# Performance work log

Hardware: AMD Instinct MI355X
Metric: run time of the kernel (lower is better)

The kernel has to match this reference:

```python
import jax, jax.numpy as jnp
import numpy as np

TOP_K = 2  # matches init_kwargs k

def setup_inputs() -> dict:
    key = jax.random.key(0)
    k1, k2 = jax.random.split(key)
    x = jax.random.normal(k1, (4, 4096, 2048), dtype=jnp.float32)
    gate_w = jax.random.normal(k2, (8, 2048), dtype=jnp.float32) * 0.02  # Linear weight [E, D]
    return {"x": x, "gate_w": gate_w}

def reference(x, gate_w):
    B, S, D = x.shape
    E = gate_w.shape[0]
    xf = x.reshape(-1, D)                              # [N, D], N = B*S
    gate_logits = jnp.einsum('nd,ed->ne', xf, gate_w)  # [N, E]
    probs = jax.nn.softmax(gate_logits.astype(jnp.float32), axis=-1)
    weights, selected = jax.lax.top_k(probs, TOP_K)    # [N, K], [N, K]
    weights = weights / jnp.sum(weights, axis=-1, keepdims=True)
    weights = weights.astype(x.dtype)
    # one_hot -> [N, K, E], permute(2,1,0) -> [E, K, N]
    expert_mask = jax.nn.one_hot(selected, E, dtype=jnp.int32).transpose(2, 1, 0)
    return weights, expert_mask, gate_logits
```

## Files before the change

### kernel.cpp

```cpp
#include <hip/hip_runtime.h>


constexpr int kN = 16384;
constexpr int kD = 2048;
constexpr int kE = 8;

__global__ __launch_bounds__(256, 4)
void moe_router_kernel(const float* __restrict__ x,
                       const float* __restrict__ gw,
                       float* __restrict__ out)
{
    const int lane = threadIdx.x & 63;
    const int wv   = threadIdx.x >> 6;
    const int n0   = blockIdx.x * 16 + wv * 4;

    const float* xr = x + (long)n0 * kD;

    float acc[4][8];
#pragma unroll
    for (int r = 0; r < 4; ++r)
#pragma unroll
        for (int e = 0; e < 8; ++e) acc[r][e] = 0.f;

#pragma unroll
    for (int it = 0; it < 8; ++it) {
        const int c = it * 256 + lane * 4;
        float4 g[8];
#pragma unroll
        for (int e = 0; e < 8; ++e)
            g[e] = *reinterpret_cast<const float4*>(gw + e * kD + c);
#pragma unroll
        for (int r = 0; r < 4; ++r) {
            const float4 xv = *reinterpret_cast<const float4*>(xr + r * kD + c);
#pragma unroll
            for (int e = 0; e < 8; ++e) {
                acc[r][e] = fmaf(xv.x, g[e].x, acc[r][e]);
                acc[r][e] = fmaf(xv.y, g[e].y, acc[r][e]);
                acc[r][e] = fmaf(xv.z, g[e].z, acc[r][e]);
                acc[r][e] = fmaf(xv.w, g[e].w, acc[r][e]);
            }
        }
    }

#pragma unroll
    for (int r = 0; r < 4; ++r)
#pragma unroll
        for (int e = 0; e < 8; ++e) {
            float v = acc[r][e];
            v += __shfl_xor(v, 1);
            v += __shfl_xor(v, 2);
            v += __shfl_xor(v, 4);
            v += __shfl_xor(v, 8);
            v += __shfl_xor(v, 16);
            v += __shfl_xor(v, 32);
            acc[r][e] = v;
        }

    float* out_w = out;
    float* out_m = out + 2 * kN;
    float* out_l = out + 2 * kN + 2 * kE * kN;

    auto load_row = [&](int r, float* le) {
#pragma unroll
        for (int e = 0; e < 8; ++e) {
            float v = acc[0][e];
            v = (r == 1) ? acc[1][e] : v;
            v = (r == 2) ? acc[2][e] : v;
            v = (r == 3) ? acc[3][e] : v;
            le[e] = v;
        }
    };
    auto top2 = [](const float* le, int& s0, int& s1) {
        float b0 = le[0]; s0 = 0;
#pragma unroll
        for (int e = 1; e < 8; ++e)
            if (le[e] > b0) { b0 = le[e]; s0 = e; }
        float b1 = -3.4e38f; s1 = (s0 == 0) ? 1 : 0;
#pragma unroll
        for (int e = 0; e < 8; ++e)
            if (e != s0 && le[e] > b1) { b1 = le[e]; s1 = e; }
    };

    {
        const int rm = lane & 3;
        const int km = (lane >> 2) & 1;
        const int em = lane >> 3;
        float le[8]; load_row(rm, le);
        int s0, s1; top2(le, s0, s1);
        const int sel = km ? s1 : s0;
        out_m[(long)em * (2 * kN) + (long)km * kN + (n0 + rm)] =
            (sel == em) ? 1.0f : 0.0f;
    }

    if (lane < 8) {
        const int rw = lane >> 1;
        const int kw = lane & 1;
        float le[8]; load_row(rw, le);
        int s0, s1; top2(le, s0, s1);
        float v0 = le[0], v1 = le[0];
#pragma unroll
        for (int e = 1; e < 8; ++e) {
            v0 = (e == s0) ? le[e] : v0;
            v1 = (e == s1) ? le[e] : v1;
        }
        const float d  = expf(v1 - v0);
        const float w0 = 1.0f / (1.0f + d);
        out_w[(long)(n0 + rw) * 2 + kw] = kw ? (d * w0) : w0;
    }

    if (lane < 32) {
        const int rl = lane >> 3;
        const int el = lane & 7;
        float le[8]; load_row(rl, le);
        float v = le[0];
#pragma unroll
        for (int e = 1; e < 8; ++e)
            v = (e == el) ? le[e] : v;
        out_l[(long)(n0 + rl) * 8 + el] = v;
    }
}

extern "C" void kernel_launch(void* const* d_in, const int* in_sizes, int n_in,
                              void* d_out, int out_size, void* d_ws, size_t ws_size,
                              hipStream_t stream)
{
    (void)in_sizes; (void)n_in; (void)d_ws; (void)ws_size; (void)out_size;
    const float* x  = (const float*)d_in[0];
    const float* gw = (const float*)d_in[1];
    float* out = (float*)d_out;

    dim3 grid(kN / 16);
    dim3 block(256);
    moe_router_kernel<<<grid, block, 0, stream>>>(x, gw, out);
}
```

Measured before the change: 37.97 us.

## Use nontemporal x loads, disable main-loop unroll, and transpose-reduce partial sums

The x rows are now loaded with nontemporal vector loads hoisted ahead of the gate-weight loads, and the main loop is no longer unrolled. The cross-lane reduction becomes a recursive-halving transpose that leaves each lane holding all 8 logits for one row, so the shuffle count drops and each lane computes top-2 only once. The aim is to cut shuffle/ALU overhead and cache pollution in this bandwidth-bound kernel. The rolled loop may expose load latency because fewer loads are in flight.

```diff
diff --git a/kernel.cpp b/kernel.cpp
--- a/kernel.cpp
+++ b/kernel.cpp
@@ -1,9 +1,12 @@
 #include <hip/hip_runtime.h>
+#include <math.h>
 
 
 constexpr int kN = 16384;
 constexpr int kD = 2048;
 constexpr int kE = 8;
+
+using f4 = __attribute__((ext_vector_type(4))) float;
 
 __global__ __launch_bounds__(256, 4)
 void moe_router_kernel(const float* __restrict__ x,
@@ -22,101 +25,94 @@
 #pragma unroll
         for (int e = 0; e < 8; ++e) acc[r][e] = 0.f;
 
-#pragma unroll
+#pragma unroll 1
     for (int it = 0; it < 8; ++it) {
         const int c = it * 256 + lane * 4;
-        float4 g[8];
+        f4 xv[4];
+#pragma unroll
+        for (int r = 0; r < 4; ++r)
+            xv[r] = __builtin_nontemporal_load(
+                reinterpret_cast<const f4*>(xr + (long)r * kD + c));
+        f4 g[8];
 #pragma unroll
         for (int e = 0; e < 8; ++e)
-            g[e] = *reinterpret_cast<const float4*>(gw + e * kD + c);
+            g[e] = *reinterpret_cast<const f4*>(gw + e * kD + c);
 #pragma unroll
-        for (int r = 0; r < 4; ++r) {
-            const float4 xv = *reinterpret_cast<const float4*>(xr + r * kD + c);
+        for (int r = 0; r < 4; ++r)
 #pragma unroll
             for (int e = 0; e < 8; ++e) {
-                acc[r][e] = fmaf(xv.x, g[e].x, acc[r][e]);
-                acc[r][e] = fmaf(xv.y, g[e].y, acc[r][e]);
-                acc[r][e] = fmaf(xv.z, g[e].z, acc[r][e]);
-                acc[r][e] = fmaf(xv.w, g[e].w, acc[r][e]);
+                acc[r][e] = fmaf(xv[r].x, g[e].x, acc[r][e]);
+                acc[r][e] = fmaf(xv[r].y, g[e].y, acc[r][e]);
+                acc[r][e] = fmaf(xv[r].z, g[e].z, acc[r][e]);
+                acc[r][e] = fmaf(xv[r].w, g[e].w, acc[r][e]);
             }
-        }
     }
 
+    const int rsel = lane & 1;
+    float a2[2][8];
 #pragma unroll
-    for (int r = 0; r < 4; ++r)
+    for (int j = 0; j < 2; ++j)
 #pragma unroll
         for (int e = 0; e < 8; ++e) {
-            float v = acc[r][e];
-            v += __shfl_xor(v, 1);
-            v += __shfl_xor(v, 2);
-            v += __shfl_xor(v, 4);
-            v += __shfl_xor(v, 8);
-            v += __shfl_xor(v, 16);
-            v += __shfl_xor(v, 32);
-            acc[r][e] = v;
+            const float mine  = rsel ? acc[2 * j + 1][e] : acc[2 * j][e];
+            const float other = rsel ? acc[2 * j][e]     : acc[2 * j + 1][e];
+            a2[j][e] = mine + __shfl_xor(other, 1);
         }
+    const int sel = (lane >> 1) & 1;
+    float a1[8];
+#pragma unroll
+    for (int e = 0; e < 8; ++e) {
+        const float mine  = sel ? a2[1][e] : a2[0][e];
+        const float other = sel ? a2[0][e] : a2[1][e];
+        a1[e] = mine + __shfl_xor(other, 2);
+    }
+#pragma unroll
+    for (int e = 0; e < 8; ++e) {
+        float v = a1[e];
+        v += __shfl_xor(v, 4);
+        v += __shfl_xor(v, 8);
+        v += __shfl_xor(v, 16);
+        v += __shfl_xor(v, 32);
+        a1[e] = v;
+    }
+
+    int s0 = 0; float b0 = a1[0];
+#pragma unroll
+    for (int e = 1; e < 8; ++e)
+        if (a1[e] > b0) { b0 = a1[e]; s0 = e; }
+    int s1 = 0; float b1 = -3.4e38f;
+#pragma unroll
+    for (int e = 0; e < 8; ++e) {
+        const bool t = (e != s0) && (a1[e] > b1);
+        b1 = t ? a1[e] : b1;
+        s1 = t ? e : s1;
+    }
+    const float d  = expf(b1 - b0);
+    const float w0 = 1.0f / (1.0f + d);
+    const float w1 = d * w0;
 
     float* out_w = out;
     float* out_m = out + 2 * kN;
     float* out_l = out + 2 * kN + 2 * kE * kN;
 
-    auto load_row = [&](int r, float* le) {
-#pragma unroll
-        for (int e = 0; e < 8; ++e) {
-            float v = acc[0][e];
-            v = (r == 1) ? acc[1][e] : v;
-            v = (r == 2) ? acc[2][e] : v;
-            v = (r == 3) ? acc[3][e] : v;
-            le[e] = v;
-        }
-    };
-    auto top2 = [](const float* le, int& s0, int& s1) {
-        float b0 = le[0]; s0 = 0;
+    const int row = lane & 3;
+    const int q   = lane >> 2;
+
+    {
+        const int em = lane >> 3;
+        const int km = (lane >> 2) & 1;
+        const int ss = km ? s1 : s0;
+        out_m[(long)em * (2 * kN) + (long)km * kN + (n0 + row)] =
+            (ss == em) ? 1.0f : 0.0f;
+    }
+    if (lane < 8)
+        out_w[(long)(n0 + row) * 2 + q] = q ? w1 : w0;
+    if (lane < 32) {
+        float v = a1[0];
 #pragma unroll
         for (int e = 1; e < 8; ++e)
-            if (le[e] > b0) { b0 = le[e]; s0 = e; }
-        float b1 = -3.4e38f; s1 = (s0 == 0) ? 1 : 0;
-#pragma unroll
-        for (int e = 0; e < 8; ++e)
-            if (e != s0 && le[e] > b1) { b1 = le[e]; s1 = e; }
-    };
-
-    {
-        const int rm = lane & 3;
-        const int km = (lane >> 2) & 1;
-        const int em = lane >> 3;
-        float le[8]; load_row(rm, le);
-        int s0, s1; top2(le, s0, s1);
-        const int sel = km ? s1 : s0;
-        out_m[(long)em * (2 * kN) + (long)km * kN + (n0 + rm)] =
-            (sel == em) ? 1.0f : 0.0f;
-    }
-
-    if (lane < 8) {
-        const int rw = lane >> 1;
-        const int kw = lane & 1;
-        float le[8]; load_row(rw, le);
-        int s0, s1; top2(le, s0, s1);
-        float v0 = le[0], v1 = le[0];
-#pragma unroll
-        for (int e = 1; e < 8; ++e) {
-            v0 = (e == s0) ? le[e] : v0;
-            v1 = (e == s1) ? le[e] : v1;
-        }
-        const float d  = expf(v1 - v0);
-        const float w0 = 1.0f / (1.0f + d);
-        out_w[(long)(n0 + rw) * 2 + kw] = kw ? (d * w0) : w0;
-    }
-
-    if (lane < 32) {
-        const int rl = lane >> 3;
-        const int el = lane & 7;
-        float le[8]; load_row(rl, le);
-        float v = le[0];
-#pragma unroll
-        for (int e = 1; e < 8; ++e)
-            v = (e == el) ? le[e] : v;
-        out_l[(long)(n0 + rl) * 8 + el] = v;
+            v = (q == e) ? a1[e] : v;
+        out_l[(long)(n0 + row) * 8 + q] = v;
     }
 }
 
```

After: 32.65 us. 1.16x faster.
